# Kernel tuning notes

Measured on AMD Instinct MI355X. Metric: run time of the kernel, lower is better.

Reference implementation:

```python
import jax, jax.numpy as jnp
from jax import lax
import numpy as np

WINDOW_SIZE = 11
K1 = 0.01
K2 = 0.03
EPS = 1e-06


def _box_filter(x, k):
    """Depthwise uniform box filter with SAME (zero) padding, matching F.conv2d(..., groups=C)."""
    c = x.shape[1]
    kernel = jnp.full((c, 1, k, k), 1.0 / (k * k), dtype=x.dtype)  # [C,1,k,k]
    pad = k // 2
    return lax.conv_general_dilated(
        x, kernel,
        window_strides=(1, 1),
        padding=[(pad, pad), (pad, pad)],
        dimension_numbers=("NCHW", "OIHW", "NCHW"),
        feature_group_count=c,
    )


def setup_inputs() -> dict:
    key = jax.random.key(0)
    k1, k2 = jax.random.split(key)
    shape = (32, 3, 512, 512)
    pred = jax.random.uniform(k1, shape, dtype=jnp.float32)
    target = jax.random.uniform(k2, shape, dtype=jnp.float32)
    return {"pred": pred, "target": target}


def reference(pred, target):
    k = WINDOW_SIZE
    mu_p = _box_filter(pred, k)
    mu_t = _box_filter(target, k)
    sigma_p = _box_filter(pred * pred, k) - mu_p * mu_p
    sigma_t = _box_filter(target * target, k) - mu_t * mu_t
    sigma_x = _box_filter(pred * target, k) - mu_p * mu_t
    sigma_p = jnp.maximum(sigma_p, 0.0)
    sigma_t = jnp.maximum(sigma_t, 0.0)

    # per (batch, channel) dynamic range over spatial dims
    dyn_max = jnp.max(jnp.maximum(pred, target), axis=(-2, -1), keepdims=True)
    dyn_min = jnp.min(jnp.minimum(pred, target), axis=(-2, -1), keepdims=True)
    data_range = jnp.maximum(dyn_max - dyn_min, EPS)
    c1 = (K1 * data_range) ** 2
    c2 = (K2 * data_range) ** 2

    numerator = (2.0 * mu_p * mu_t + c1) * (2.0 * sigma_x + c2)
    denominator = (mu_p * mu_p + mu_t * mu_t + c1) * (sigma_p + sigma_t + c2)
    ssim_map = numerator / (denominator + EPS)
    loss_map = jnp.maximum((1.0 - ssim_map) * 0.5, 0.0)
    return jnp.mean(loss_map)
```

## Files before the change

kernel.cpp:

```cpp
#include <hip/hip_runtime.h>

constexpr int Wd = 512;
constexpr int PLANE = 512 * 512;

typedef float v2f __attribute__((ext_vector_type(2)));

__device__ __forceinline__ float dpp_up1(float x) {
    return __int_as_float(__builtin_amdgcn_update_dpp(
        0, __float_as_int(x), 0x138, 0xF, 0xF, true));
}
__device__ __forceinline__ float dpp_down1(float x) {
    return __int_as_float(__builtin_amdgcn_update_dpp(
        0, __float_as_int(x), 0x130, 0xF, 0xF, true));
}

__device__ __forceinline__ float fast_rcp(float x) {
    return __builtin_amdgcn_rcpf(x);
}

__global__ __launch_bounds__(256) void minmax_part(const float* __restrict__ pred,
                                                   const float* __restrict__ targ,
                                                   float* __restrict__ pmx,
                                                   float* __restrict__ pmn) {
    int bx = blockIdx.x;
    int plane = bx >> 4, seg = bx & 15;
    size_t base = (size_t)plane * PLANE + (size_t)seg * 16384;
    const float4* p4 = reinterpret_cast<const float4*>(pred + base);
    const float4* t4 = reinterpret_cast<const float4*>(targ + base);
    float mx = -3.0e38f, mn = 3.0e38f;
    #pragma unroll 4
    for (int i = threadIdx.x; i < 4096; i += 256) {
        float4 a = p4[i], b = t4[i];
        mx = fmaxf(mx, fmaxf(fmaxf(fmaxf(a.x, b.x), fmaxf(a.y, b.y)),
                             fmaxf(fmaxf(a.z, b.z), fmaxf(a.w, b.w))));
        mn = fminf(mn, fminf(fminf(fminf(a.x, b.x), fminf(a.y, b.y)),
                             fminf(fminf(a.z, b.z), fminf(a.w, b.w))));
    }
    #pragma unroll
    for (int off = 32; off; off >>= 1) {
        mx = fmaxf(mx, __shfl_down(mx, off));
        mn = fminf(mn, __shfl_down(mn, off));
    }
    __shared__ float smx[4], smn[4];
    int wid = threadIdx.x >> 6, lane = threadIdx.x & 63;
    if (lane == 0) { smx[wid] = mx; smn[wid] = mn; }
    __syncthreads();
    if (threadIdx.x == 0) {
        pmx[bx] = fmaxf(fmaxf(smx[0], smx[1]), fmaxf(smx[2], smx[3]));
        pmn[bx] = fminf(fminf(smn[0], smn[1]), fminf(smn[2], smn[3]));
    }
}

__global__ __launch_bounds__(128) void ssim_main(const float* __restrict__ pred,
                                                 const float* __restrict__ targ,
                                                 const float* __restrict__ pmx,
                                                 const float* __restrict__ pmn,
                                                 float* __restrict__ parts) {
    __shared__ float red[2];
    int bx = blockIdx.x;
    int plane = bx >> 3, tile = bx & 7;
    int wid = threadIdx.x >> 6, c = threadIdx.x & 63;

    float mx = -3.0e38f, mn = 3.0e38f;
    #pragma unroll
    for (int s = 0; s < 16; ++s) {
        mx = fmaxf(mx, pmx[plane * 16 + s]);
        mn = fminf(mn, pmn[plane * 16 + s]);
    }
    float dr = fmaxf(mx - mn, 1e-6f);
    const float c1 = 1.4641f * dr * dr;
    const float c2 = 13.1769f * dr * dr;
    const v2f c1v = {c1, c1}, c2v = {c2, c2};
    const v2f k121 = {121.0f, 121.0f};

    const float* Pg = pred + (size_t)plane * PLANE;
    const float* Tg = targ + (size_t)plane * PLANE;
    int r0 = tile * 64 + wid * 32;

    v2f vsP[4], vsT[4], vsQQ[4], vsPT[4];
    #pragma unroll
    for (int j = 0; j < 4; ++j) { vsP[j] = 0; vsT[j] = 0; vsQQ[j] = 0; vsPT[j] = 0; }

    struct RowData { float4 a0, a1, b0, b1; };

    auto load_row = [&](int r) -> RowData {
        int rc = min(max(r, 0), 511);
        const float4* prow = reinterpret_cast<const float4*>(Pg + (size_t)rc * Wd);
        const float4* trow = reinterpret_cast<const float4*>(Tg + (size_t)rc * Wd);
        RowData d;
        d.a0 = prow[2 * c]; d.a1 = prow[2 * c + 1];
        d.b0 = trow[2 * c]; d.b1 = trow[2 * c + 1];
        return d;
    };

    auto acc_w = [&](const RowData& d, float w) {
        v2f wv = {w, w};
        v2f pa[4] = {{d.a0.x, d.a0.y}, {d.a0.z, d.a0.w}, {d.a1.x, d.a1.y}, {d.a1.z, d.a1.w}};
        v2f tb[4] = {{d.b0.x, d.b0.y}, {d.b0.z, d.b0.w}, {d.b1.x, d.b1.y}, {d.b1.z, d.b1.w}};
        #pragma unroll
        for (int j = 0; j < 4; ++j) {
            vsP[j] += wv * pa[j];
            vsT[j] += wv * tb[j];
            v2f q = pa[j] * pa[j] + tb[j] * tb[j];
            vsQQ[j] += wv * q;
            v2f pt = pa[j] * tb[j];
            vsPT[j] += wv * pt;
        }
    };

    auto hsum = [&](const v2f v[4], v2f H[4]) {
        float P0 = v[0].x;
        float P1 = P0 + v[0].y;
        float P2 = P1 + v[1].x;
        float P3 = P2 + v[1].y;
        float P4 = P3 + v[2].x;
        float P5 = P4 + v[2].y;
        float P6 = P5 + v[3].x;
        float T  = P6 + v[3].y;
        float Tm  = dpp_up1(T);
        float Pm2 = dpp_up1(P2);
        float Pm3 = dpp_up1(P3);
        float Pm4 = dpp_up1(P4);
        float Pm5 = dpp_up1(P5);
        float Pm6 = dpp_up1(P6);
        float Pp0 = dpp_down1(P0);
        float Pp1 = dpp_down1(P1);
        float Pp2 = dpp_down1(P2);
        float Pp3 = dpp_down1(P3);
        float Pp4 = dpp_down1(P4);
        H[0].x = (Tm - Pm2) + P5;
        H[0].y = (Tm - Pm3) + P6;
        H[1].x = (Tm - Pm4) + T;
        H[1].y = (Tm - Pm5) + (T + Pp0);
        H[2].x = (Tm - Pm6) + (T + Pp1);
        H[2].y = T + Pp2;
        H[3].x = (T - P0) + Pp3;
        H[3].y = (T - P1) + Pp4;
    };

    v2f lsum2 = {0.0f, 0.0f};

    auto valid = [&](int r) -> float { return ((unsigned)r < 512u) ? 1.0f : 0.0f; };

    auto body = [&](int it, const RowData& E, const RowData& Lv, RowData& En, RowData& Ln) {
        En = load_row(r0 + it + 6);
        Ln = load_row(r0 + it - 4);

        acc_w(E, valid(r0 + it + 5));

        v2f H[4][4];
        hsum(vsP,  H[0]);
        hsum(vsT,  H[1]);
        hsum(vsQQ, H[2]);
        hsum(vsPT, H[3]);

        #pragma unroll
        for (int j = 0; j < 4; ++j) {
            v2f A = H[0][j], B = H[1][j];
            v2f AB = A * B, A2 = A * A, B2 = B * B;
            v2f t4 = k121 * H[3][j] - AB;
            v2f num = (2.0f * AB + c1v) * (2.0f * t4 + c2v);
            v2f ss = k121 * H[2][j] - A2 - B2;
            ss.x = fmaxf(ss.x, 0.0f); ss.y = fmaxf(ss.y, 0.0f);
            v2f den = (A2 + B2 + c1v) * (ss + c2v);
            float s0 = num.x * fast_rcp(den.x + 214.358881f);
            float s1 = num.y * fast_rcp(den.y + 214.358881f);
            v2f loss = {fmaxf((1.0f - s0) * 0.5f, 0.0f),
                        fmaxf((1.0f - s1) * 0.5f, 0.0f)};
            lsum2 += loss;
        }
        acc_w(Lv, -valid(r0 + it - 5));
    };

    {
        RowData D0 = load_row(r0 - 5), D1 = load_row(r0 - 4), D2 = load_row(r0 - 3),
                D3 = load_row(r0 - 2), D4 = load_row(r0 - 1);
        acc_w(D0, valid(r0 - 5)); acc_w(D1, valid(r0 - 4)); acc_w(D2, valid(r0 - 3));
        acc_w(D3, valid(r0 - 2)); acc_w(D4, valid(r0 - 1));
        RowData D5 = load_row(r0 + 0), D6 = load_row(r0 + 1), D7 = load_row(r0 + 2),
                D8 = load_row(r0 + 3), D9 = load_row(r0 + 4);
        acc_w(D5, 1.0f); acc_w(D6, 1.0f); acc_w(D7, 1.0f);
        acc_w(D8, 1.0f); acc_w(D9, 1.0f);
    }

    RowData E0 = load_row(r0 + 5);
    RowData L0 = load_row(r0 - 5);
    RowData E1, L1;

    #pragma unroll 1
    for (int it = 0; it < 32; it += 2) {
        body(it,     E0, L0, E1, L1);
        body(it + 1, E1, L1, E0, L0);
    }

    float lsum = lsum2.x + lsum2.y;
    #pragma unroll
    for (int off = 32; off; off >>= 1) lsum += __shfl_down(lsum, off);
    if (c == 0) red[wid] = lsum;
    __syncthreads();
    if (threadIdx.x == 0) parts[bx] = red[0] + red[1];
}

__global__ void finish(const float* __restrict__ parts, float* __restrict__ out,
                       int n, float invN) {
    float s = 0.0f;
    for (int i = threadIdx.x; i < n; i += 256) s += parts[i];
    #pragma unroll
    for (int off = 32; off; off >>= 1) s += __shfl_down(s, off);
    __shared__ float sw[4];
    int wid = threadIdx.x >> 6, lane = threadIdx.x & 63;
    if (lane == 0) sw[wid] = s;
    __syncthreads();
    if (threadIdx.x == 0) out[0] = ((sw[0] + sw[1]) + (sw[2] + sw[3])) * invN;
}

extern "C" void kernel_launch(void* const* d_in, const int* in_sizes, int n_in,
                              void* d_out, int out_size, void* d_ws, size_t ws_size,
                              hipStream_t stream) {
    const float* pred = (const float*)d_in[0];
    const float* targ = (const float*)d_in[1];
    float* out = (float*)d_out;
    int planes = in_sizes[0] / PLANE;
    int Gm = planes * 16;
    int Gs = planes * 8;

    float* ws   = (float*)d_ws;
    float* pmx  = ws;
    float* pmn  = ws + Gm;
    float* prts = ws + 2 * Gm;

    minmax_part<<<Gm, 256, 0, stream>>>(pred, targ, pmx, pmn);
    ssim_main<<<Gs, 128, 0, stream>>>(pred, targ, pmx, pmn, prts);
    float invN = 1.0f / ((float)planes * (float)PLANE);
    finish<<<1, 256, 0, stream>>>(prts, out, Gs, invN);
}
```

Measured before the change: 102.6 us.

## Fuse final reduction into SSIM kernel via last-block atomic counter

Removes the separate finish kernel: each ssim_main block writes its partial, bumps an atomic counter, and the last block to arrive sums all partials and writes the output. This is meant to save one kernel launch and its tail latency, but adds a hipMemsetAsync to reset the counter each call. Separately, the min/max pass now uses 512-thread blocks over larger segments, halving its grid size and the number of partials ssim_main reads.

New measurement: 123.8 us. +20.6%, slower.

```diff
diff --git a/kernel.cpp b/kernel.cpp
--- a/kernel.cpp
+++ b/kernel.cpp
@@ -18,18 +18,18 @@
     return __builtin_amdgcn_rcpf(x);
 }
 
-__global__ __launch_bounds__(256) void minmax_part(const float* __restrict__ pred,
+__global__ __launch_bounds__(512) void minmax_part(const float* __restrict__ pred,
                                                    const float* __restrict__ targ,
                                                    float* __restrict__ pmx,
                                                    float* __restrict__ pmn) {
     int bx = blockIdx.x;
-    int plane = bx >> 4, seg = bx & 15;
-    size_t base = (size_t)plane * PLANE + (size_t)seg * 16384;
+    int plane = bx >> 3, seg = bx & 7;
+    size_t base = (size_t)plane * PLANE + (size_t)seg * 32768;
     const float4* p4 = reinterpret_cast<const float4*>(pred + base);
     const float4* t4 = reinterpret_cast<const float4*>(targ + base);
     float mx = -3.0e38f, mn = 3.0e38f;
-    #pragma unroll 4
-    for (int i = threadIdx.x; i < 4096; i += 256) {
+    #pragma unroll 8
+    for (int i = threadIdx.x; i < 8192; i += 512) {
         float4 a = p4[i], b = t4[i];
         mx = fmaxf(mx, fmaxf(fmaxf(fmaxf(a.x, b.x), fmaxf(a.y, b.y)),
                              fmaxf(fmaxf(a.z, b.z), fmaxf(a.w, b.w))));
@@ -41,13 +41,19 @@
         mx = fmaxf(mx, __shfl_down(mx, off));
         mn = fminf(mn, __shfl_down(mn, off));
     }
-    __shared__ float smx[4], smn[4];
+    __shared__ float smx[8], smn[8];
     int wid = threadIdx.x >> 6, lane = threadIdx.x & 63;
     if (lane == 0) { smx[wid] = mx; smn[wid] = mn; }
     __syncthreads();
     if (threadIdx.x == 0) {
-        pmx[bx] = fmaxf(fmaxf(smx[0], smx[1]), fmaxf(smx[2], smx[3]));
-        pmn[bx] = fminf(fminf(smn[0], smn[1]), fminf(smn[2], smn[3]));
+        float gmx = smx[0], gmn = smn[0];
+        #pragma unroll
+        for (int w = 1; w < 8; ++w) {
+            gmx = fmaxf(gmx, smx[w]);
+            gmn = fminf(gmn, smn[w]);
+        }
+        pmx[bx] = gmx;
+        pmn[bx] = gmn;
     }
 }
 
@@ -55,7 +61,10 @@
                                                  const float* __restrict__ targ,
                                                  const float* __restrict__ pmx,
                                                  const float* __restrict__ pmn,
-                                                 float* __restrict__ parts) {
+                                                 float* __restrict__ parts,
+                                                 unsigned int* __restrict__ counter,
+                                                 float* __restrict__ out,
+                                                 int nblocks, float invN) {
     __shared__ float red[2];
     int bx = blockIdx.x;
     int plane = bx >> 3, tile = bx & 7;
@@ -63,9 +72,9 @@
 
     float mx = -3.0e38f, mn = 3.0e38f;
     #pragma unroll
-    for (int s = 0; s < 16; ++s) {
-        mx = fmaxf(mx, pmx[plane * 16 + s]);
-        mn = fminf(mn, pmn[plane * 16 + s]);
+    for (int s = 0; s < 8; ++s) {
+        mx = fmaxf(mx, pmx[plane * 8 + s]);
+        mn = fminf(mn, pmn[plane * 8 + s]);
     }
     float dr = fmaxf(mx - mn, 1e-6f);
     const float c1 = 1.4641f * dr * dr;
@@ -198,20 +207,26 @@
     for (int off = 32; off; off >>= 1) lsum += __shfl_down(lsum, off);
     if (c == 0) red[wid] = lsum;
     __syncthreads();
-    if (threadIdx.x == 0) parts[bx] = red[0] + red[1];
-}
-
-__global__ void finish(const float* __restrict__ parts, float* __restrict__ out,
-                       int n, float invN) {
-    float s = 0.0f;
-    for (int i = threadIdx.x; i < n; i += 256) s += parts[i];
-    #pragma unroll
-    for (int off = 32; off; off >>= 1) s += __shfl_down(s, off);
-    __shared__ float sw[4];
-    int wid = threadIdx.x >> 6, lane = threadIdx.x & 63;
-    if (lane == 0) sw[wid] = s;
+
+    __shared__ bool amLast;
+    if (threadIdx.x == 0) {
+        parts[bx] = red[0] + red[1];
+        __threadfence();
+        unsigned int old = atomicAdd(counter, 1u);
+        amLast = (old == (unsigned int)(nblocks - 1));
+    }
     __syncthreads();
-    if (threadIdx.x == 0) out[0] = ((sw[0] + sw[1]) + (sw[2] + sw[3])) * invN;
+
+    if (amLast) {
+        __threadfence();
+        float s = 0.0f;
+        for (int i = threadIdx.x; i < nblocks; i += 128) s += parts[i];
+        #pragma unroll
+        for (int off = 32; off; off >>= 1) s += __shfl_down(s, off);
+        if (c == 0) red[wid] = s;
+        __syncthreads();
+        if (threadIdx.x == 0) out[0] = (red[0] + red[1]) * invN;
+    }
 }
 
 extern "C" void kernel_launch(void* const* d_in, const int* in_sizes, int n_in,
@@ -221,16 +236,16 @@
     const float* targ = (const float*)d_in[1];
     float* out = (float*)d_out;
     int planes = in_sizes[0] / PLANE;
-    int Gm = planes * 16;
-    int Gs = planes * 8;
-
-    float* ws   = (float*)d_ws;
-    float* pmx  = ws;
-    float* pmn  = ws + Gm;
-    float* prts = ws + 2 * Gm;
-
-    minmax_part<<<Gm, 256, 0, stream>>>(pred, targ, pmx, pmn);
-    ssim_main<<<Gs, 128, 0, stream>>>(pred, targ, pmx, pmn, prts);
+    int G = planes * 8;
+
+    float* ws = (float*)d_ws;
+    unsigned int* counter = (unsigned int*)ws;
+    float* pmx  = ws + 1;
+    float* pmn  = ws + 1 + G;
+    float* prts = ws + 1 + 2 * G;
+
+    hipMemsetAsync(counter, 0, sizeof(unsigned int), stream);
+    minmax_part<<<G, 512, 0, stream>>>(pred, targ, pmx, pmn);
     float invN = 1.0f / ((float)planes * (float)PLANE);
-    finish<<<1, 256, 0, stream>>>(prts, out, Gs, invN);
-}
+    ssim_main<<<G, 128, 0, stream>>>(pred, targ, pmx, pmn, prts, counter, out, G, invN);
+}
```
